# Performance work log

Measured on AMD Instinct MI355X. Metric: run time of the kernel, lower is better.

Reference implementation:

```python
import jax, jax.numpy as jnp
from jax import lax
import numpy as np

B, D_IN, L, D, K, DS = 8, 16, 4096, 512, 4, 4
BLOCKS = (1, 2, 3, 4)          # block sizes, all offset 0 (max_block_size=4)
PAD_MULT = 12                  # lcm(1,2,3,4)


def setup_inputs() -> dict:
    key = jax.random.key(0)
    ks = jax.random.split(key, 5)
    return {
        "x": jax.random.normal(ks[0], (B, D_IN, L), jnp.float32),
        "conv_w": jax.random.normal(ks[1], (D, D_IN, K), jnp.float32) * 0.05,
        "conv_b": jax.random.normal(ks[2], (D,), jnp.float32) * 0.02,
        "score_w": jax.random.normal(ks[3], (D,), jnp.float32) * 0.02,
        "score_b": jax.random.normal(ks[4], (1,), jnp.float32) * 0.02,
    }


def reference(x, conv_w, conv_b, score_w, score_b):
    # pos_conv: Conv1d(padding='same', k=4). Torch 'same' with even kernel pads
    # left=(k-1)//2=1, right=2.
    h = lax.conv_general_dilated(x, conv_w, (1,), [(1, 2)],
                                 dimension_numbers=('NCH', 'OIH', 'NCH'))
    h = jnp.transpose(h, (0, 2, 1)) + conv_b            # [B, L, D]

    Np = -(-L // PAD_MULT) * PAD_MULT                   # pad seq to multiple of 12
    h = jnp.pad(h, ((0, 0), (0, Np - L), (0, 0)))       # [B, Np, D]

    # per-block-size mean pooling, then broadcast back to char resolution
    reprs = []
    for m in BLOCKS:
        r = h.reshape(B, Np // m, m, D).mean(axis=2)    # [B, Np/m, D]
        reprs.append(jnp.repeat(r, m, axis=1))          # [B, Np, D]
    br = jnp.stack(reprs, axis=2)                       # [B, Np, nb, D]

    # score each block representation, softmax over block sizes
    scores = jnp.einsum('bnmd,d->bnm', br, score_w) + score_b[0]
    scores = jax.nn.softmax(scores, axis=2)             # [B, Np, nb]

    # consensus attention across positions over the nb-dim score vectors
    sim = jnp.einsum('bim,bjm->bij', scores, scores)    # [B, Np, Np]
    attn = jax.nn.softmax(sim, axis=-1)
    scores = jnp.einsum('bij,bjm->bim', attn, scores)   # [B, Np, nb]

    # weighted sum of block reprs
    xo = jnp.einsum('bnmd,bnm->bnd', br, scores)        # [B, Np, D]

    mlen = -(-L // DS) * DS                              # 4096 (== L here)
    char_x = xo[:, :mlen]
    xd = char_x.reshape(B, mlen // DS, DS, D).mean(axis=2)  # [B, L/DS, D]
    return char_x[:, :L], xd
```

## Files before the change

kernel.cpp:

```cpp
#include <hip/hip_runtime.h>
#include <hip/hip_bf16.h>

#define B_ 8
#define DIN 16
#define L_ 4096
#define D_ 512
#define NP 4104
#define NG 342
#define JSP 32
#define JCH 129
#define SPAN 48
#define NSPAN 86
#define WSTRIDE 133

__device__ __forceinline__ unsigned short f2bf(float f) {
  unsigned int u = __float_as_uint(f);
  unsigned int r = (u + 0x7fffu + ((u >> 16) & 1u)) >> 16;
  return (unsigned short)r;
}
__device__ __forceinline__ float bf2f(unsigned int u) {
  return __uint_as_float(u << 16);
}

__device__ __constant__ float D5[6] = {0.9999544f, 1.0005163f, 0.4975827f,
                                       0.1726558f, 0.0334570f, 0.0140872f};
__device__ __constant__ float FACT[6] = {1.f, 1.f, 2.f, 6.f, 24.f, 120.f};

__global__ __launch_bounds__(256) void k_uprep(
    const float* __restrict__ cw, const float* __restrict__ cb,
    const float* __restrict__ sw, float* __restrict__ us) {
  __shared__ float red[4][64];
  __shared__ float red2[64];
  int t = threadIdx.x;
  int p = t & 63, chunk = t >> 6;
  float s = 0.f;
  for (int d = chunk * 128; d < chunk * 128 + 128; ++d)
    s = fmaf(sw[d], cw[((size_t)d << 6) + p], s);
  red[chunk][p] = s;
  if (t < 64) {
    float pc = 0.f;
    for (int j = 0; j < 8; ++j) pc = fmaf(sw[t + 64 * j], cb[t + 64 * j], pc);
    red2[t] = pc;
  }
  __syncthreads();
  if (t < 64) us[t] = red[0][t] + red[1][t] + red[2][t] + red[3][t];
  if (t == 0) {
    float c0 = 0.f;
    for (int j = 0; j < 64; ++j) c0 += red2[j];
    us[64] = c0;
  }
}

__global__ __launch_bounds__(192) void k_scores(
    const float* __restrict__ x, const float* __restrict__ us,
    const float* __restrict__ sb, unsigned short* __restrict__ s0) {
  __shared__ float xs[DIN * 195];
  __shared__ float ul[65];
  __shared__ float tb[192];
  int bid = blockIdx.x;
  int b = bid / 22, blk = bid - b * 22;
  int base0 = blk * 192;
  int t = threadIdx.x;
  const float* xb = x + (size_t)b * DIN * L_;
  for (int q = t; q < DIN * 195; q += 192) {
    int i = q / 195, c = q - i * 195;
    int nx = base0 - 1 + c;
    xs[q] = (nx >= 0 && nx < L_) ? xb[i * L_ + nx] : 0.f;
  }
  if (t < 65) ul[t] = us[t];
  __syncthreads();
  int n = base0 + t;
  float tv = 0.f;
  if (n < L_) {
    tv = ul[64];
    for (int i = 0; i < DIN; ++i) {
#pragma unroll
      for (int k = 0; k < 4; ++k)
        tv = fmaf(xs[i * 195 + t + k], ul[(i << 2) + k], tv);
    }
  }
  tb[t] = tv;
  __syncthreads();
  if (n < NP) {
    float t1 = tb[t];
    int e2 = t & ~1;
    float t2 = 0.5f * (tb[e2] + tb[e2 + 1]);
    int e3 = (t / 3) * 3;
    float t3 = (1.f / 3.f) * (tb[e3] + tb[e3 + 1] + tb[e3 + 2]);
    int e4 = t & ~3;
    float t4 = 0.25f * (tb[e4] + tb[e4 + 1] + tb[e4 + 2] + tb[e4 + 3]);
    float sbv = sb[0];
    float c0s = t1 + sbv, c1s = t2 + sbv, c2s = t3 + sbv, c3s = t4 + sbv;
    float mx = fmaxf(fmaxf(c0s, c1s), fmaxf(c2s, c3s));
    float e0 = __expf(c0s - mx), e1 = __expf(c1s - mx);
    float e2f = __expf(c2s - mx), e3f = __expf(c3s - mx);
    float inv = 1.f / (e0 + e1 + e2f + e3f);
    ushort4 ov;
    ov.x = f2bf(e0 * inv); ov.y = f2bf(e1 * inv);
    ov.z = f2bf(e2f * inv); ov.w = f2bf(e3f * inv);
    *reinterpret_cast<ushort4*>(&s0[(((size_t)b * NP) + n) << 2]) = ov;
  }
}

__global__ __launch_bounds__(256) void k_moment(
    const unsigned short* __restrict__ s0, float* __restrict__ Mpart) {
  __shared__ float sv[JCH][4];
  __shared__ float ls[JCH][4];
  __shared__ float mp[4][128][5];
  int bid = blockIdx.x;
  int js = bid & 31;
  int b = bid >> 5;
  int t = threadIdx.x;
  int lane = t & 63, wv = t >> 6;
  int jlo = js * JCH;
  int cnt = NP - jlo; if (cnt > JCH) cnt = JCH;

  const ushort4* sp = reinterpret_cast<const ushort4*>(s0) + (size_t)b * NP + jlo;
  for (int r = t; r < cnt; r += 256) {
    ushort4 u = sp[r];
    float v0 = bf2f(u.x), v1 = bf2f(u.y), v2 = bf2f(u.z), v3 = bf2f(u.w);
    sv[r][0] = v0; sv[r][1] = v1; sv[r][2] = v2; sv[r][3] = v3;
    ls[r][0] = __log2f(v0); ls[r][1] = __log2f(v1);
    ls[r][2] = __log2f(v2); ls[r][3] = __log2f(v3);
  }
  int f1 = lane, f2 = lane + 64;
  float e1a = 0.f, e1b = 0.f, e1c = 0.f, e1d = 0.f;
  float e2a = 0.f, e2b = 0.f, e2c = 0.f, e2d = 0.f;
  {
    int f = 0;
    for (int a = 0; a <= 5; ++a)
      for (int b2 = 0; b2 <= 5 - a; ++b2)
        for (int c = 0; c <= 5 - a - b2; ++c)
          for (int d2 = 0; d2 <= 5 - a - b2 - c; ++d2) {
            if (f == f1) { e1a = a; e1b = b2; e1c = c; e1d = d2; }
            if (f == f2) { e2a = a; e2b = b2; e2c = c; e2d = d2; }
            ++f;
          }
  }
  __syncthreads();
  float acc1[5] = {0.f, 0.f, 0.f, 0.f, 0.f};
  float acc2[5] = {0.f, 0.f, 0.f, 0.f, 0.f};
  for (int jj = wv; jj < cnt; jj += 4) {
    float4 lv = *reinterpret_cast<float4*>(&ls[jj][0]);
    float4 vv = *reinterpret_cast<float4*>(&sv[jj][0]);
    float t1 = e1a * lv.x;
    t1 = fmaf(e1b, lv.y, t1);
    t1 = fmaf(e1c, lv.z, t1);
    t1 = fmaf(e1d, lv.w, t1);
    float t2 = e2a * lv.x;
    t2 = fmaf(e2b, lv.y, t2);
    t2 = fmaf(e2c, lv.z, t2);
    t2 = fmaf(e2d, lv.w, t2);
    float m1 = exp2f(t1);
    float m2 = exp2f(t2);
    acc1[0] = fmaf(m1, vv.x, acc1[0]);
    acc1[1] = fmaf(m1, vv.y, acc1[1]);
    acc1[2] = fmaf(m1, vv.z, acc1[2]);
    acc1[3] = fmaf(m1, vv.w, acc1[3]);
    acc1[4] += m1;
    acc2[0] = fmaf(m2, vv.x, acc2[0]);
    acc2[1] = fmaf(m2, vv.y, acc2[1]);
    acc2[2] = fmaf(m2, vv.z, acc2[2]);
    acc2[3] = fmaf(m2, vv.w, acc2[3]);
    acc2[4] += m2;
  }
#pragma unroll
  for (int c = 0; c < 5; ++c) {
    mp[wv][lane][c] = acc1[c];
    mp[wv][lane + 64][c] = acc2[c];
  }
  __syncthreads();
  if (t < 630) {
    int f = t / 5, c = t - f * 5;
    float s = mp[0][f][c] + mp[1][f][c] + mp[2][f][c] + mp[3][f][c];
    int fa = 0, fb = 0, fc = 0, fd = 0;
    {
      int ff = 0;
      for (int a = 0; a <= 5; ++a)
        for (int b2 = 0; b2 <= 5 - a; ++b2)
          for (int cc = 0; cc <= 5 - a - b2; ++cc)
            for (int d2 = 0; d2 <= 5 - a - b2 - cc; ++d2) {
              if (ff == f) { fa = a; fb = b2; fc = cc; fd = d2; }
              ++ff;
            }
    }
    int k = fa + fb + fc + fd;
    float w = D5[k] * FACT[k] / (FACT[fa] * FACT[fb] * FACT[fc] * FACT[fd]);
    Mpart[((size_t)(b * 32 + js)) * 640 + t] = w * s;
  }
}

__global__ __launch_bounds__(256) void k_apply(
    const unsigned short* __restrict__ s0, const float* __restrict__ Mpart,
    float* __restrict__ s2) {
  __shared__ float M[128 * 8];
  int bid = blockIdx.x;
  int b = bid / 17, ch = bid - b * 17;
  int t = threadIdx.x;
  for (int e = t; e < 630; e += 256) {
    float s = 0.f;
#pragma unroll 4
    for (int js = 0; js < JSP; ++js)
      s += Mpart[((size_t)(b * 32 + js)) * 640 + e];
    int f = e / 5, c = e - f * 5;
    M[f * 8 + c] = s;
  }
  __syncthreads();
  int i = ch * 256 + t;
  if (i >= NP) return;
  ushort4 u = reinterpret_cast<const ushort4*>(s0)[(size_t)b * NP + i];
  float s_0 = bf2f(u.x), s_1 = bf2f(u.y), s_2 = bf2f(u.z), s_3 = bf2f(u.w);
  float a0 = 0.f, a1 = 0.f, a2 = 0.f, a3 = 0.f, az = 0.f;
  int f = 0;
  float pa = 1.f;
#pragma unroll
  for (int a = 0; a <= 5; ++a) {
    float pb = pa;
#pragma unroll
    for (int b2 = 0; b2 <= 5 - a; ++b2) {
      float pc = pb;
#pragma unroll
      for (int c = 0; c <= 5 - a - b2; ++c) {
        float run = pc;
#pragma unroll
        for (int d2 = 0; d2 <= 5 - a - b2 - c; ++d2) {
          const float* mf = &M[f * 8];
          float4 m4 = *reinterpret_cast<const float4*>(mf);
          a0 = fmaf(run, m4.x, a0);
          a1 = fmaf(run, m4.y, a1);
          a2 = fmaf(run, m4.z, a2);
          a3 = fmaf(run, m4.w, a3);
          az = fmaf(run, mf[4], az);
          run *= s_3;
          ++f;
        }
        pc *= s_2;
      }
      pb *= s_1;
    }
    pa *= s_0;
  }
  float inv = 1.f / az;
  reinterpret_cast<float4*>(s2)[(size_t)b * NP + i] =
      make_float4(a0 * inv, a1 * inv, a2 * inv, a3 * inv);
}

__global__ __launch_bounds__(256, 4) void k_fused(
    const float* __restrict__ x, const float* __restrict__ cw,
    const float* __restrict__ cb, const float* __restrict__ s2,
    float* __restrict__ out) {
  __shared__ float ws_w[64 * WSTRIDE];
  __shared__ float ws_x[DIN * 52];
  __shared__ float ss[4][12][4];
  int bid = blockIdx.x;
  int dtile = bid & 3;
  int span = (bid >> 2) % NSPAN;
  int b = bid / (4 * NSPAN);
  int n0 = span * SPAN;
  int d0 = dtile * 128;
  int g0 = n0 / 12;
  int tid = threadIdx.x;

  for (int q = tid; q < 128 * 16; q += 256) {
    int dd = q >> 4, qq = (q & 15) << 2;
    int dpw = dd >> 1;
    float4 wv = *reinterpret_cast<const float4*>(cw + ((size_t)(d0 + dd) << 6) + qq);
    *reinterpret_cast<float4*>(&ws_w[dpw * WSTRIDE + (dd & 1) * 64 + qq]) = wv;
  }
  const float* xb = x + (size_t)b * DIN * L_;
  for (int q = tid; q < DIN * 52; q += 256) {
    int i = q / 52, c = q - i * 52;
    int nx = n0 - 1 + c;
    ws_x[q] = (c < 51 && nx >= 0 && nx < L_) ? xb[i * L_ + nx] : 0.f;
  }
  if (tid < 192) {
    int gg = tid / 48, r = tid - gg * 48;
    int g = g0 + gg;
    ((float*)ss)[tid] = (g < NG) ? s2[((size_t)b * NP + g * 12) * 4 + r] : 0.f;
  }
  __syncthreads();

  int dp = tid & 63;
  int seg = tid >> 6;
  int g = g0 + seg;
  int wbase = dp * WSTRIDE;
  float acc0[12], acc1[12];
#pragma unroll
  for (int j = 0; j < 12; ++j) { acc0[j] = 0.f; acc1[j] = 0.f; }

  for (int i = 0; i < DIN; ++i) {
    float4 wv0 = *reinterpret_cast<const float4*>(&ws_w[wbase + (i << 2)]);
    float4 wv1 = *reinterpret_cast<const float4*>(&ws_w[wbase + 64 + (i << 2)]);
    const float* xp = &ws_x[i * 52 + seg * 12];
    float4 xv0 = *reinterpret_cast<const float4*>(xp);
    float4 xv1 = *reinterpret_cast<const float4*>(xp + 4);
    float4 xv2 = *reinterpret_cast<const float4*>(xp + 8);
    float4 xv3 = *reinterpret_cast<const float4*>(xp + 12);
    float xr[16] = {xv0.x, xv0.y, xv0.z, xv0.w, xv1.x, xv1.y, xv1.z, xv1.w,
                    xv2.x, xv2.y, xv2.z, xv2.w, xv3.x, xv3.y, xv3.z, xv3.w};
#pragma unroll
    for (int j = 0; j < 12; ++j) {
      float a0 = acc0[j], a1 = acc1[j];
      a0 = fmaf(wv0.x, xr[j], a0);
      a0 = fmaf(wv0.y, xr[j + 1], a0);
      a0 = fmaf(wv0.z, xr[j + 2], a0);
      a0 = fmaf(wv0.w, xr[j + 3], a0);
      a1 = fmaf(wv1.x, xr[j], a1);
      a1 = fmaf(wv1.y, xr[j + 1], a1);
      a1 = fmaf(wv1.z, xr[j + 2], a1);
      a1 = fmaf(wv1.w, xr[j + 3], a1);
      acc0[j] = a0; acc1[j] = a1;
    }
  }
  if (g >= NG) return;

  int d = d0 + (dp << 1);
  float cb0 = cb[d], cb1 = cb[d + 1];
  int base = g * 12;
  float hv0[12], hv1[12];
#pragma unroll
  for (int j = 0; j < 12; ++j) {
    int n = base + j;
    if (n < L_) { hv0[j] = acc0[j] + cb0; hv1[j] = acc1[j] + cb1; }
    else { hv0[j] = 0.f; hv1[j] = 0.f; }
  }
  float P20[6], P21[6], P30[4], P31[4], P40[3], P41[3];
#pragma unroll
  for (int q = 0; q < 6; ++q) {
    P20[q] = 0.5f * (hv0[2 * q] + hv0[2 * q + 1]);
    P21[q] = 0.5f * (hv1[2 * q] + hv1[2 * q + 1]);
  }
#pragma unroll
  for (int q = 0; q < 4; ++q) {
    P30[q] = (1.f / 3.f) * (hv0[3 * q] + hv0[3 * q + 1] + hv0[3 * q + 2]);
    P31[q] = (1.f / 3.f) * (hv1[3 * q] + hv1[3 * q + 1] + hv1[3 * q + 2]);
  }
#pragma unroll
  for (int q = 0; q < 3; ++q) {
    P40[q] = 0.25f * (hv0[4 * q] + hv0[4 * q + 1] + hv0[4 * q + 2] + hv0[4 * q + 3]);
    P41[q] = 0.25f * (hv1[4 * q] + hv1[4 * q + 1] + hv1[4 * q + 2] + hv1[4 * q + 3]);
  }
  float* outc = out;
  float* outd = out + (size_t)B_ * L_ * D_;
  float xq0[3] = {0.f, 0.f, 0.f}, xq1[3] = {0.f, 0.f, 0.f};
#pragma unroll
  for (int j = 0; j < 12; ++j) {
    float w0 = ss[seg][j][0], w1 = ss[seg][j][1];
    float w2 = ss[seg][j][2], w3 = ss[seg][j][3];
    float v0 = w0 * hv0[j] + w1 * P20[j >> 1] + w2 * P30[j / 3] + w3 * P40[j >> 2];
    float v1 = w0 * hv1[j] + w1 * P21[j >> 1] + w2 * P31[j / 3] + w3 * P41[j >> 2];
    int n = base + j;
    if (n < L_) {
      float2 o; o.x = v0; o.y = v1;
      *reinterpret_cast<float2*>(&outc[((size_t)b * L_ + n) * D_ + d]) = o;
    }
    xq0[j >> 2] += v0; xq1[j >> 2] += v1;
  }
#pragma unroll
  for (int q = 0; q < 3; ++q) {
    int r = 3 * g + q;
    if (r < 1024) {
      float2 o; o.x = 0.25f * xq0[q]; o.y = 0.25f * xq1[q];
      *reinterpret_cast<float2*>(&outd[((size_t)b * 1024 + r) * D_ + d]) = o;
    }
  }
}

extern "C" void kernel_launch(void* const* d_in, const int* in_sizes, int n_in,
                              void* d_out, int out_size, void* d_ws, size_t ws_size,
                              hipStream_t stream) {
  const float* x = (const float*)d_in[0];
  const float* cw = (const float*)d_in[1];
  const float* cb = (const float*)d_in[2];
  const float* sw = (const float*)d_in[3];
  const float* sb = (const float*)d_in[4];
  float* out = (float*)d_out;
  char* ws = (char*)d_ws;
  size_t off = 0;
  unsigned short* s0 = (unsigned short*)(ws + off);
  off += 262656;
  float* s2 = (float*)(ws + off);
  off += 525312;
  float* Mpart = (float*)(ws + off);
  off += 655360;
  float* us = (float*)(ws + off);

  k_uprep<<<1, 256, 0, stream>>>(cw, cb, sw, us);
  k_scores<<<8 * 22, 192, 0, stream>>>(x, us, sb, s0);
  k_moment<<<B_ * JSP, 256, 0, stream>>>(s0, Mpart);
  k_apply<<<B_ * 17, 256, 0, stream>>>(s0, Mpart, s2);
  k_fused<<<B_ * NSPAN * 4, 256, 0, stream>>>(x, cw, cb, s2, out);
}
```

Before: 80.83 us.

## Merge four small prep kernels into one cooperative kernel with grid syncs

Replaces the uprep/scores/moment/apply launch chain with a single cooperative kernel of 256 blocks that separates the phases with grid.sync(). Per-block shared memory is reused across phases, and the uprep reduction is spread over 65 blocks instead of one. The old four-launch path stays as a fallback if the cooperative launch fails. It also changes the k_fused weight tile stride from 133 to 132, which can alter LDS bank conflicts. The aim is to remove launch gaps and tail idle time between small kernels, at the cost of grid-wide barrier overhead.

```diff
diff --git a/kernel.cpp b/kernel.cpp
--- a/kernel.cpp
+++ b/kernel.cpp
@@ -1,5 +1,8 @@
 #include <hip/hip_runtime.h>
 #include <hip/hip_bf16.h>
+#include <hip/hip_cooperative_groups.h>
+
+namespace cg = cooperative_groups;
 
 #define B_ 8
 #define DIN 16
@@ -11,7 +14,6 @@
 #define JCH 129
 #define SPAN 48
 #define NSPAN 86
-#define WSTRIDE 133
 
 __device__ __forceinline__ unsigned short f2bf(float f) {
   unsigned int u = __float_as_uint(f);
@@ -25,6 +27,228 @@
 __device__ __constant__ float D5[6] = {0.9999544f, 1.0005163f, 0.4975827f,
                                        0.1726558f, 0.0334570f, 0.0140872f};
 __device__ __constant__ float FACT[6] = {1.f, 1.f, 2.f, 6.f, 24.f, 120.f};
+
+__global__ __launch_bounds__(256) void k_chain(
+    const float* __restrict__ x, const float* __restrict__ cw,
+    const float* __restrict__ cb, const float* __restrict__ sw,
+    const float* __restrict__ sb, unsigned short* __restrict__ s0,
+    float* __restrict__ Mpart, float* __restrict__ us, float* __restrict__ s2) {
+  cg::grid_group grid = cg::this_grid();
+  __shared__ float pool[3648];
+  int t = threadIdx.x;
+  int vb = blockIdx.x;
+
+  if (vb < 65) {
+    float sv_;
+    if (vb < 64)
+      sv_ = sw[t] * cw[((size_t)t << 6) + vb] +
+            sw[t + 256] * cw[((size_t)(t + 256) << 6) + vb];
+    else
+      sv_ = sw[t] * cb[t] + sw[t + 256] * cb[t + 256];
+    pool[t] = sv_;
+    __syncthreads();
+    if (t < 64) pool[t] += pool[t + 64] + pool[t + 128] + pool[t + 192];
+    __syncthreads();
+    if (t == 0) {
+      float s = 0.f;
+      for (int j = 0; j < 64; ++j) s += pool[j];
+      us[vb] = s;
+    }
+  }
+  grid.sync();
+
+  if (vb < 176) {
+    float* xs = pool;
+    float* ul = pool + 3120;
+    float* tb = pool + 3200;
+    int b = vb / 22, blk = vb - b * 22;
+    int base0 = blk * 192;
+    const float* xb = x + (size_t)b * DIN * L_;
+    for (int q = t; q < DIN * 195; q += 256) {
+      int i = q / 195, c = q - i * 195;
+      int nx = base0 - 1 + c;
+      xs[q] = (nx >= 0 && nx < L_) ? xb[i * L_ + nx] : 0.f;
+    }
+    if (t < 65) ul[t] = us[t];
+    __syncthreads();
+    if (t < 192) {
+      int n = base0 + t;
+      float tv = 0.f;
+      if (n < L_) {
+        tv = ul[64];
+        for (int i = 0; i < DIN; ++i) {
+#pragma unroll
+          for (int k = 0; k < 4; ++k)
+            tv = fmaf(xs[i * 195 + t + k], ul[(i << 2) + k], tv);
+        }
+      }
+      tb[t] = tv;
+    }
+    __syncthreads();
+    if (t < 192) {
+      int n = base0 + t;
+      if (n < NP) {
+        float t1 = tb[t];
+        int e2 = t & ~1;
+        float t2 = 0.5f * (tb[e2] + tb[e2 + 1]);
+        int e3 = (t / 3) * 3;
+        float t3 = (1.f / 3.f) * (tb[e3] + tb[e3 + 1] + tb[e3 + 2]);
+        int e4 = t & ~3;
+        float t4 = 0.25f * (tb[e4] + tb[e4 + 1] + tb[e4 + 2] + tb[e4 + 3]);
+        float sbv = sb[0];
+        float c0s = t1 + sbv, c1s = t2 + sbv, c2s = t3 + sbv, c3s = t4 + sbv;
+        float mx = fmaxf(fmaxf(c0s, c1s), fmaxf(c2s, c3s));
+        float e0 = __expf(c0s - mx), e1 = __expf(c1s - mx);
+        float e2f = __expf(c2s - mx), e3f = __expf(c3s - mx);
+        float inv = 1.f / (e0 + e1 + e2f + e3f);
+        ushort4 ov;
+        ov.x = f2bf(e0 * inv); ov.y = f2bf(e1 * inv);
+        ov.z = f2bf(e2f * inv); ov.w = f2bf(e3f * inv);
+        *reinterpret_cast<ushort4*>(&s0[(((size_t)b * NP) + n) << 2]) = ov;
+      }
+    }
+  }
+  grid.sync();
+
+  {
+    float (*sv)[4] = (float(*)[4])(pool);
+    float (*ls)[4] = (float(*)[4])(pool + 520);
+    float* mp = pool + 1040;
+    int js = vb & 31;
+    int b = vb >> 5;
+    int lane = t & 63, wv = t >> 6;
+    int jlo = js * JCH;
+    int cnt = NP - jlo; if (cnt > JCH) cnt = JCH;
+    const ushort4* sp = reinterpret_cast<const ushort4*>(s0) + (size_t)b * NP + jlo;
+    for (int r = t; r < cnt; r += 256) {
+      ushort4 u = sp[r];
+      float v0 = bf2f(u.x), v1 = bf2f(u.y), v2 = bf2f(u.z), v3 = bf2f(u.w);
+      sv[r][0] = v0; sv[r][1] = v1; sv[r][2] = v2; sv[r][3] = v3;
+      ls[r][0] = __log2f(v0); ls[r][1] = __log2f(v1);
+      ls[r][2] = __log2f(v2); ls[r][3] = __log2f(v3);
+    }
+    int f1 = lane, f2 = lane + 64;
+    float e1a = 0.f, e1b = 0.f, e1c = 0.f, e1d = 0.f;
+    float e2a = 0.f, e2b = 0.f, e2c = 0.f, e2d = 0.f;
+    {
+      int f = 0;
+      for (int a = 0; a <= 5; ++a)
+        for (int b2 = 0; b2 <= 5 - a; ++b2)
+          for (int c = 0; c <= 5 - a - b2; ++c)
+            for (int d2 = 0; d2 <= 5 - a - b2 - c; ++d2) {
+              if (f == f1) { e1a = a; e1b = b2; e1c = c; e1d = d2; }
+              if (f == f2) { e2a = a; e2b = b2; e2c = c; e2d = d2; }
+              ++f;
+            }
+    }
+    __syncthreads();
+    float acc1[5] = {0.f, 0.f, 0.f, 0.f, 0.f};
+    float acc2[5] = {0.f, 0.f, 0.f, 0.f, 0.f};
+    for (int jj = wv; jj < cnt; jj += 4) {
+      float4 lv = *reinterpret_cast<float4*>(&ls[jj][0]);
+      float4 vv = *reinterpret_cast<float4*>(&sv[jj][0]);
+      float t1 = e1a * lv.x;
+      t1 = fmaf(e1b, lv.y, t1);
+      t1 = fmaf(e1c, lv.z, t1);
+      t1 = fmaf(e1d, lv.w, t1);
+      float t2 = e2a * lv.x;
+      t2 = fmaf(e2b, lv.y, t2);
+      t2 = fmaf(e2c, lv.z, t2);
+      t2 = fmaf(e2d, lv.w, t2);
+      float m1 = exp2f(t1);
+      float m2 = exp2f(t2);
+      acc1[0] = fmaf(m1, vv.x, acc1[0]);
+      acc1[1] = fmaf(m1, vv.y, acc1[1]);
+      acc1[2] = fmaf(m1, vv.z, acc1[2]);
+      acc1[3] = fmaf(m1, vv.w, acc1[3]);
+      acc1[4] += m1;
+      acc2[0] = fmaf(m2, vv.x, acc2[0]);
+      acc2[1] = fmaf(m2, vv.y, acc2[1]);
+      acc2[2] = fmaf(m2, vv.z, acc2[2]);
+      acc2[3] = fmaf(m2, vv.w, acc2[3]);
+      acc2[4] += m2;
+    }
+    __syncthreads();
+#pragma unroll
+    for (int c = 0; c < 5; ++c) {
+      mp[wv * 640 + lane * 5 + c] = acc1[c];
+      mp[wv * 640 + (lane + 64) * 5 + c] = acc2[c];
+    }
+    __syncthreads();
+    if (t < 630) {
+      int f = t / 5, c = t - f * 5;
+      float s = mp[f * 5 + c] + mp[640 + f * 5 + c] + mp[1280 + f * 5 + c] +
+                mp[1920 + f * 5 + c];
+      int fa = 0, fb = 0, fc = 0, fd = 0;
+      {
+        int ff = 0;
+        for (int a = 0; a <= 5; ++a)
+          for (int b2 = 0; b2 <= 5 - a; ++b2)
+            for (int cc = 0; cc <= 5 - a - b2; ++cc)
+              for (int d2 = 0; d2 <= 5 - a - b2 - cc; ++d2) {
+                if (ff == f) { fa = a; fb = b2; fc = cc; fd = d2; }
+                ++ff;
+              }
+      }
+      int k = fa + fb + fc + fd;
+      float w = D5[k] * FACT[k] / (FACT[fa] * FACT[fb] * FACT[fc] * FACT[fd]);
+      Mpart[((size_t)(b * 32 + js)) * 640 + t] = w * s;
+    }
+  }
+  grid.sync();
+
+  if (vb < 136) {
+    float* M = pool;
+    int b = vb / 17, ch = vb - b * 17;
+    for (int e = t; e < 630; e += 256) {
+      float s = 0.f;
+#pragma unroll 4
+      for (int js = 0; js < JSP; ++js)
+        s += Mpart[((size_t)(b * 32 + js)) * 640 + e];
+      int f = e / 5, c = e - f * 5;
+      M[f * 8 + c] = s;
+    }
+    __syncthreads();
+    int i = ch * 256 + t;
+    if (i < NP) {
+      ushort4 u = reinterpret_cast<const ushort4*>(s0)[(size_t)b * NP + i];
+      float s_0 = bf2f(u.x), s_1 = bf2f(u.y), s_2 = bf2f(u.z), s_3 = bf2f(u.w);
+      float a0 = 0.f, a1 = 0.f, a2 = 0.f, a3 = 0.f, az = 0.f;
+      int f = 0;
+      float pa = 1.f;
+#pragma unroll
+      for (int a = 0; a <= 5; ++a) {
+        float pb = pa;
+#pragma unroll
+        for (int b2 = 0; b2 <= 5 - a; ++b2) {
+          float pc = pb;
+#pragma unroll
+          for (int c = 0; c <= 5 - a - b2; ++c) {
+            float run = pc;
+#pragma unroll
+            for (int d2 = 0; d2 <= 5 - a - b2 - c; ++d2) {
+              const float* mf = &M[f * 8];
+              float4 m4 = *reinterpret_cast<const float4*>(mf);
+              a0 = fmaf(run, m4.x, a0);
+              a1 = fmaf(run, m4.y, a1);
+              a2 = fmaf(run, m4.z, a2);
+              a3 = fmaf(run, m4.w, a3);
+              az = fmaf(run, mf[4], az);
+              run *= s_3;
+              ++f;
+            }
+            pc *= s_2;
+          }
+          pb *= s_1;
+        }
+        pa *= s_0;
+      }
+      float inv = 1.f / az;
+      reinterpret_cast<float4*>(s2)[(size_t)b * NP + i] =
+          make_float4(a0 * inv, a1 * inv, a2 * inv, a3 * inv);
+    }
+  }
+}
 
 __global__ __launch_bounds__(256) void k_uprep(
     const float* __restrict__ cw, const float* __restrict__ cb,
@@ -114,7 +338,6 @@
   int lane = t & 63, wv = t >> 6;
   int jlo = js * JCH;
   int cnt = NP - jlo; if (cnt > JCH) cnt = JCH;
-
   const ushort4* sp = reinterpret_cast<const ushort4*>(s0) + (size_t)b * NP + jlo;
   for (int r = t; r < cnt; r += 256) {
     ushort4 u = sp[r];
@@ -249,7 +472,7 @@
     const float* __restrict__ x, const float* __restrict__ cw,
     const float* __restrict__ cb, const float* __restrict__ s2,
     float* __restrict__ out) {
-  __shared__ float ws_w[64 * WSTRIDE];
+  __shared__ float ws_w[64 * 132];
   __shared__ float ws_x[DIN * 52];
   __shared__ float ss[4][12][4];
   int bid = blockIdx.x;
@@ -263,9 +486,8 @@
 
   for (int q = tid; q < 128 * 16; q += 256) {
     int dd = q >> 4, qq = (q & 15) << 2;
-    int dpw = dd >> 1;
     float4 wv = *reinterpret_cast<const float4*>(cw + ((size_t)(d0 + dd) << 6) + qq);
-    *reinterpret_cast<float4*>(&ws_w[dpw * WSTRIDE + (dd & 1) * 64 + qq]) = wv;
+    *reinterpret_cast<float4*>(&ws_w[(dd >> 1) * 132 + (dd & 1) * 64 + qq]) = wv;
   }
   const float* xb = x + (size_t)b * DIN * L_;
   for (int q = tid; q < DIN * 52; q += 256) {
@@ -283,14 +505,14 @@
   int dp = tid & 63;
   int seg = tid >> 6;
   int g = g0 + seg;
-  int wbase = dp * WSTRIDE;
   float acc0[12], acc1[12];
 #pragma unroll
   for (int j = 0; j < 12; ++j) { acc0[j] = 0.f; acc1[j] = 0.f; }
 
   for (int i = 0; i < DIN; ++i) {
-    float4 wv0 = *reinterpret_cast<const float4*>(&ws_w[wbase + (i << 2)]);
-    float4 wv1 = *reinterpret_cast<const float4*>(&ws_w[wbase + 64 + (i << 2)]);
+    const float* wp = &ws_w[dp * 132 + (i << 2)];
+    float4 wv0 = *reinterpret_cast<const float4*>(wp);
+    float4 wv1 = *reinterpret_cast<const float4*>(wp + 64);
     const float* xp = &ws_x[i * 52 + seg * 12];
     float4 xv0 = *reinterpret_cast<const float4*>(xp);
     float4 xv1 = *reinterpret_cast<const float4*>(xp + 4);
@@ -385,9 +607,15 @@
   off += 655360;
   float* us = (float*)(ws + off);
 
-  k_uprep<<<1, 256, 0, stream>>>(cw, cb, sw, us);
-  k_scores<<<8 * 22, 192, 0, stream>>>(x, us, sb, s0);
-  k_moment<<<B_ * JSP, 256, 0, stream>>>(s0, Mpart);
-  k_apply<<<B_ * 17, 256, 0, stream>>>(s0, Mpart, s2);
+  void* args[] = {(void*)&x, (void*)&cw, (void*)&cb, (void*)&sw, (void*)&sb,
+                  (void*)&s0, (void*)&Mpart, (void*)&us, (void*)&s2};
+  hipError_t cerr = hipLaunchCooperativeKernel((const void*)k_chain, dim3(256),
+                                               dim3(256), args, 0, stream);
+  if (cerr != hipSuccess) {
+    k_uprep<<<1, 256, 0, stream>>>(cw, cb, sw, us);
+    k_scores<<<8 * 22, 192, 0, stream>>>(x, us, sb, s0);
+    k_moment<<<B_ * JSP, 256, 0, stream>>>(s0, Mpart);
+    k_apply<<<B_ * 17, 256, 0, stream>>>(s0, Mpart, s2);
+  }
   k_fused<<<B_ * NSPAN * 4, 256, 0, stream>>>(x, cw, cb, s2, out);
 }
```

New measurement: 164.0 us. +102.9%, slower.
